# Performance work log

Measured on AMD Instinct MI355X. Metric: run time of the kernel, lower is better.

## Reference

```python
import jax, jax.numpy as jnp
import numpy as np
from functools import partial

BATCH, SEQ = 2, 2048
D_MODEL, D_INNER, D_XB = 2048, 4096, 1024
HEADDIM, D_STATE = 64, 64
NHEADS = D_INNER // HEADDIM      # 64
NKV = D_XB // HEADDIM            # 16
REP = NHEADS // NKV              # 4
INTER = 8192
EPS = 1e-5
D_IN_PROJ = D_INNER + D_XB + D_XB + D_INNER + NHEADS  # z, x, B, C, dt


def setup_inputs() -> dict:
    key = jax.random.key(0)
    ks = jax.random.split(key, 8)
    g = lambda k, shape, s: (jax.random.normal(k, shape, jnp.float32) * s)
    return {
        "hidden_states": g(ks[0], (BATCH, SEQ, D_MODEL), 1.0),
        "ln_w": jnp.ones((D_MODEL,), jnp.float32),
        "ln_b": jnp.zeros((D_MODEL,), jnp.float32),
        "in_proj_w": g(ks[1], (D_IN_PROJ, D_MODEL), 0.02),
        "dt_bias": jax.random.uniform(ks[2], (NHEADS,), jnp.float32, -4.0, 0.0),
        "A_log": jnp.log(jnp.arange(1, NHEADS + 1, dtype=jnp.float32)),
        "Dp": jnp.ones((NHEADS,), jnp.float32),
        "norm_w": jnp.ones((D_INNER,), jnp.float32),
        "out_proj_w": g(ks[3], (D_MODEL, D_INNER), 0.02),
        "fc1_w": g(ks[4], (INTER, D_MODEL), 0.02),
        "fc1_b": jnp.zeros((INTER,), jnp.float32),
        "fc2_w": g(ks[5], (D_MODEL, INTER), 0.02),
        "fc2_b": jnp.zeros((D_MODEL,), jnp.float32),
    }


def _layernorm(x, w, b):
    mu = x.mean(-1, keepdims=True)
    var = ((x - mu) ** 2).mean(-1, keepdims=True)
    return (x - mu) * jax.lax.rsqrt(var + EPS) * w + b


def _ssd_scan(xh, dt, A, Bh, Ch):
    # xh: (b,l,h,p)  dt: (b,l,h)  A: (h,)  Bh,Ch: (b,l,h,n)
    dA = jnp.exp(dt * A)  # (b,l,h) discrete decay
    to_l = lambda t: jnp.moveaxis(t, 1, 0)  # time-major for scan

    def step(state, inp):
        dA_t, dt_t, x_t, B_t, C_t = inp
        state = state * dA_t[:, :, None, None] + jnp.einsum(
            "bh,bhp,bhn->bhpn", dt_t, x_t, B_t)
        y = jnp.einsum("bhpn,bhn->bhp", state, C_t)
        return state, y

    state0 = jnp.zeros((xh.shape[0], NHEADS, HEADDIM, D_STATE), xh.dtype)
    _, ys = jax.lax.scan(step, state0, (to_l(dA), to_l(dt), to_l(xh), to_l(Bh), to_l(Ch)))
    return jnp.moveaxis(ys, 0, 1)  # (b,l,h,p)


def reference(hidden_states, ln_w, ln_b, in_proj_w, dt_bias, A_log, Dp,
              norm_w, out_proj_w, fc1_w, fc1_b, fc2_w, fc2_b):
    residual = hidden_states
    h = _layernorm(hidden_states, ln_w, ln_b)

    # ---- Mamba2 branch ----
    zxbcdt = h @ in_proj_w.T  # (b,l,D_IN_PROJ)
    z, x, Bm, Cm, dt = jnp.split(
        zxbcdt, np.cumsum([D_INNER, D_XB, D_XB, D_INNER]).tolist(), axis=-1)
    b, l = h.shape[0], h.shape[1]
    dt = jax.nn.softplus(dt + dt_bias)               # (b,l,nheads)
    A = -jnp.exp(A_log)                              # (nheads,)
    # GQA-style repeat of x (values) and B (keys) from NKV to NHEADS groups
    xh = jnp.repeat(x.reshape(b, l, NKV, HEADDIM), REP, axis=2)   # (b,l,h,p)
    Bh = jnp.repeat(Bm.reshape(b, l, NKV, D_STATE), REP, axis=2)  # (b,l,h,n)
    Ch = Cm.reshape(b, l, NHEADS, D_STATE)                        # (b,l,h,n)

    y = _ssd_scan(xh, dt, A, Bh, Ch) + Dp[None, None, :, None] * xh
    yf = y.reshape(b, l, D_INNER)
    # gated RMSNorm (norm_before_gate=False): gate first, then rmsnorm
    yf = yf * jax.nn.silu(z)
    yf = yf * jax.lax.rsqrt((yf * yf).mean(-1, keepdims=True) + EPS) * norm_w
    mamba_out = yf @ out_proj_w.T

    # ---- Phi MLP branch (parallel, shares the layernormed input) ----
    mlp = jax.nn.gelu(h @ fc1_w.T + fc1_b, approximate=True) @ fc2_w.T + fc2_b

    # resid_dropout is identity in eval mode
    return mamba_out + mlp + residual
```

## Files before the change

kernel.cpp:

```cpp
#include <hip/hip_runtime.h>
#include <hip/hip_bf16.h>

#define BATCH 2
#define SEQ   2048
#define DMODEL 2048
#define DINNER 4096
#define DXB   1024
#define NHEADS 64
#define NKV   16
#define HEADDIM 64
#define DSTATE 64
#define INTER 8192
#define DINPROJ 10304
#define ROWS  (BATCH*SEQ)
#define NC    32
#define EPSV  1e-5f

typedef short short8 __attribute__((ext_vector_type(8)));
typedef float f32x4 __attribute__((ext_vector_type(4)));

typedef const __attribute__((address_space(1))) unsigned int cg_u32;
typedef __attribute__((address_space(3))) unsigned int ls_u32;

static __device__ __forceinline__ void gll16(const void* g, void* l) {
    __builtin_amdgcn_global_load_lds((cg_u32*)g, (ls_u32*)l, 16, 0, 0);
}

static __device__ __forceinline__ unsigned short f2bf(float f) {
    unsigned int u = __float_as_uint(f);
    unsigned int r = (u + 0x7fffu + ((u >> 16) & 1u)) >> 16;
    return (unsigned short)r;
}
static __device__ __forceinline__ float bf2f(unsigned short h) {
    return __uint_as_float(((unsigned int)h) << 16);
}

__global__ __launch_bounds__(256) void convk(const float* __restrict__ in,
                                             unsigned short* __restrict__ out, int n4) {
    int stride = gridDim.x * blockDim.x;
    for (int i = blockIdx.x * blockDim.x + threadIdx.x; i < n4; i += stride) {
        float4 v = ((const float4*)in)[i];
        ushort4 o;
        o.x = f2bf(v.x); o.y = f2bf(v.y); o.z = f2bf(v.z); o.w = f2bf(v.w);
        ((ushort4*)out)[i] = o;
    }
}

__global__ __launch_bounds__(256) void ln_kernel(const float* __restrict__ x,
                                                 const float* __restrict__ w,
                                                 const float* __restrict__ b,
                                                 unsigned short* __restrict__ hout) {
    int row = blockIdx.x;
    int t = threadIdx.x;
    const float* xr = x + (size_t)row * DMODEL;
    float v[8];
    float4 v0 = *(const float4*)&xr[t * 8];
    float4 v1 = *(const float4*)&xr[t * 8 + 4];
    v[0]=v0.x; v[1]=v0.y; v[2]=v0.z; v[3]=v0.w; v[4]=v1.x; v[5]=v1.y; v[6]=v1.z; v[7]=v1.w;
    float s = 0.f, s2 = 0.f;
    #pragma unroll
    for (int i = 0; i < 8; ++i) { s += v[i]; s2 += v[i]*v[i]; }
    #pragma unroll
    for (int off = 1; off < 64; off <<= 1) { s += __shfl_xor(s, off); s2 += __shfl_xor(s2, off); }
    __shared__ float sa[4], sb[4];
    int lane = t & 63, wv = t >> 6;
    if (lane == 0) { sa[wv] = s; sb[wv] = s2; }
    __syncthreads();
    s = sa[0]+sa[1]+sa[2]+sa[3];
    s2 = sb[0]+sb[1]+sb[2]+sb[3];
    float mu = s / DMODEL;
    float var = s2 / DMODEL - mu * mu;
    float sc = rsqrtf(var + EPSV);
    unsigned short* ho = hout + (size_t)row * DMODEL + t * 8;
    #pragma unroll
    for (int i = 0; i < 8; ++i) {
        int d = t * 8 + i;
        ho[i] = f2bf((v[i] - mu) * sc * w[d] + b[d]);
    }
}

#define SLOTSZ 49152
template <int EPI>
__global__ __launch_bounds__(512, 2) void gemm_p(
    const unsigned short* __restrict__ A, const unsigned short* __restrict__ B,
    int M, int N, int K, int nby,
    float* __restrict__ outF, unsigned short* __restrict__ outH,
    const float* __restrict__ bias, const float* __restrict__ add1,
    const float* __restrict__ add2) {
    __shared__ __align__(16) char smem[3 * SLOTSZ];
    int t = threadIdx.x, lane = t & 63, w = t >> 6;
    int nwg = gridDim.x, cpx = nwg >> 3;
    int logical = (blockIdx.x & 7) * cpx + (blockIdx.x >> 3);
    int by = logical % nby, bx = logical / nby;
    int brow = by * 128, bcol = bx * 256;
    int wr = w >> 2, wc = w & 3;
    int wrb = wr * 64, wcb = wc * 64;

    int lr8 = lane >> 3;
    int lch = ((lane & 7) ^ lr8) << 3;
    const unsigned short* pa[2];
    #pragma unroll
    for (int j = 0; j < 2; ++j)
        pa[j] = A + (size_t)(brow + w * 16 + j * 8 + lr8) * K + lch;
    const unsigned short* pb[4];
    #pragma unroll
    for (int j = 0; j < 4; ++j) {
        int r = bcol + w * 32 + j * 8 + lr8;
        if (r > N - 1) r = N - 1;
        pb[j] = B + (size_t)r * K + lch;
    }
    auto stageA = [&](int slot, int j) {
        gll16(pa[j], smem + slot * SLOTSZ + (w * 16 + j * 8) * 128);
        pa[j] += 64;
    };
    auto stageB = [&](int slot, int j) {
        gll16(pb[j], smem + slot * SLOTSZ + 16384 + (w * 32 + j * 8) * 128);
        pb[j] += 64;
    };

    int arow = lane & 15;
    int swz0 = (((lane >> 4) ^ (lane & 7)) << 4);

    f32x4 acc[4][4] = {};
    const int NT = K >> 6;
    #pragma unroll
    for (int j = 0; j < 2; ++j) stageA(0, j);
    #pragma unroll
    for (int j = 0; j < 4; ++j) stageB(0, j);
    #pragma unroll
    for (int j = 0; j < 2; ++j) stageA(1, j);
    #pragma unroll
    for (int j = 0; j < 4; ++j) stageB(1, j);

    int slot = 0, slot2 = 2;
    for (int kt = 0; kt < NT; ++kt) {
        if (kt + 1 < NT) { asm volatile("s_waitcnt vmcnt(6)" ::: "memory"); }
        else             { asm volatile("s_waitcnt vmcnt(0)" ::: "memory"); }
        __builtin_amdgcn_s_barrier();
        asm volatile("" ::: "memory");
        const char* Ab = smem + slot * SLOTSZ;
        const char* Bb = Ab + 16384;
        bool st = (kt + 2 < NT);
        short8 af[4], bfv[4];
        #pragma unroll
        for (int f = 0; f < 4; ++f)
            af[f] = *(const short8*)(Ab + (wrb + f * 16 + arow) * 128 + swz0);
        #pragma unroll
        for (int n = 0; n < 4; ++n)
            bfv[n] = *(const short8*)(Bb + (wcb + n * 16 + arow) * 128 + swz0);
        if (st) { stageA(slot2, 0); stageA(slot2, 1); stageB(slot2, 0); }
        __builtin_amdgcn_s_setprio(1);
        #pragma unroll
        for (int f = 0; f < 4; ++f)
            #pragma unroll
            for (int n = 0; n < 4; ++n)
                acc[f][n] = __builtin_amdgcn_mfma_f32_16x16x32_bf16(af[f], bfv[n], acc[f][n], 0, 0, 0);
        __builtin_amdgcn_s_setprio(0);
        #pragma unroll
        for (int f = 0; f < 4; ++f)
            af[f] = *(const short8*)(Ab + (wrb + f * 16 + arow) * 128 + (swz0 ^ 64));
        #pragma unroll
        for (int n = 0; n < 4; ++n)
            bfv[n] = *(const short8*)(Bb + (wcb + n * 16 + arow) * 128 + (swz0 ^ 64));
        if (st) { stageB(slot2, 1); stageB(slot2, 2); stageB(slot2, 3); }
        __builtin_amdgcn_s_setprio(1);
        #pragma unroll
        for (int f = 0; f < 4; ++f)
            #pragma unroll
            for (int n = 0; n < 4; ++n)
                acc[f][n] = __builtin_amdgcn_mfma_f32_16x16x32_bf16(af[f], bfv[n], acc[f][n], 0, 0, 0);
        __builtin_amdgcn_s_setprio(0);
        slot  = (slot  == 2) ? 0 : slot + 1;
        slot2 = (slot2 == 2) ? 0 : slot2 + 1;
    }

    int rlane = (lane >> 4) << 2, clane = lane & 15;
    #pragma unroll
    for (int f = 0; f < 4; ++f) {
        #pragma unroll
        for (int n = 0; n < 4; ++n) {
            int col = bcol + wcb + n * 16 + clane;
            if (col < N) {
                #pragma unroll
                for (int j = 0; j < 4; ++j) {
                    int row = brow + wrb + f * 16 + rlane + j;
                    size_t idx = (size_t)row * N + col;
                    float v = acc[f][n][j];
                    if constexpr (EPI == 0) {
                        outF[idx] = v;
                    } else if constexpr (EPI == 1) {
                        v += bias[col];
                        float g = 0.5f * v * (1.f + tanhf(0.7978845608f * (v + 0.044715f * v * v * v)));
                        outH[idx] = f2bf(g);
                    } else if constexpr (EPI == 2) {
                        outF[idx] = v + bias[col] + add1[idx] + add2[idx];
                    } else {
                        outH[idx] = f2bf(v);
                    }
                }
            }
        }
    }
}

static __device__ __forceinline__ void mm64(const unsigned short* Al, const unsigned short* Bl,
                                            f32x4* acc, int w, int lane) {
    int lr = lane & 15, kg = (lane >> 4) << 3;
    #pragma unroll
    for (int ks = 0; ks < 2; ++ks) {
        short8 a = *(const short8*)&Al[(w * 16 + lr) * 64 + ks * 32 + kg];
        #pragma unroll
        for (int fn = 0; fn < 4; ++fn) {
            short8 bb = *(const short8*)&Bl[(fn * 16 + lr) * 64 + ks * 32 + kg];
            acc[fn] = __builtin_amdgcn_mfma_f32_16x16x32_bf16(a, bb, acc[fn], 0, 0, 0);
        }
    }
}

__global__ __launch_bounds__(256) void chunk_front(const unsigned short* __restrict__ zx,
                                                   const float* __restrict__ dt_bias,
                                                   const float* __restrict__ A_log,
                                                   float* __restrict__ pcum,
                                                   unsigned short* __restrict__ ybuf,
                                                   unsigned short* __restrict__ Sbuf) {
    __shared__ __align__(16) unsigned short Cs[64*64], Bsr[64*64], Btr[64*64],
                                            Xtr[64*64], Xw[64*64], Wsm[64*64];
    __shared__ float dts[64], clg[64];
    int t = threadIdx.x, lane = t & 63, w = t >> 6;
    int bid = blockIdx.x;
    int c = bid & 31, h = (bid >> 5) & 63, b = bid >> 11, g = h >> 2;
    int row0 = (b << 11) + (c << 6);

    if (t < 64) {
        float raw = bf2f(zx[(size_t)(row0 + t) * DINPROJ + 10240 + h]) + dt_bias[h];
        float dt = raw > 20.f ? raw : log1pf(expf(raw));
        dts[t] = dt;
        float v = dt * (-expf(A_log[h]));
        #pragma unroll
        for (int off = 1; off < 64; off <<= 1) {
            float o = __shfl_up(v, off);
            if (lane >= off) v += o;
        }
        clg[t] = v;
        pcum[(size_t)(row0 + t) * 64 + h] = expf(v);
    }
    ushort4 xr[4];
    #pragma unroll
    for (int i = 0; i < 4; ++i) {
        int q = i * 256 + t, s = q >> 4, d4 = (q & 15) << 2;
        const unsigned short* rp = zx + (size_t)(row0 + s) * DINPROJ;
        ushort4 cv = *(const ushort4*)&rp[6144 + h * 64 + d4];
        *(ushort4*)&Cs[s * 64 + d4] = cv;
        ushort4 bv = *(const ushort4*)&rp[5120 + g * 64 + d4];
        *(ushort4*)&Bsr[s * 64 + d4] = bv;
        Btr[(d4 + 0) * 64 + s] = bv.x; Btr[(d4 + 1) * 64 + s] = bv.y;
        Btr[(d4 + 2) * 64 + s] = bv.z; Btr[(d4 + 3) * 64 + s] = bv.w;
        ushort4 xv = *(const ushort4*)&rp[4096 + g * 64 + d4];
        Xtr[(d4 + 0) * 64 + s] = xv.x; Xtr[(d4 + 1) * 64 + s] = xv.y;
        Xtr[(d4 + 2) * 64 + s] = xv.z; Xtr[(d4 + 3) * 64 + s] = xv.w;
        xr[i] = xv;
    }
    __syncthreads();
    float cl63 = clg[63];
    #pragma unroll
    for (int i = 0; i < 4; ++i) {
        int q = i * 256 + t, s = q >> 4, d4 = (q & 15) << 2;
        float ws = dts[s] * expf(cl63 - clg[s]);
        Xw[(d4 + 0) * 64 + s] = f2bf(bf2f(xr[i].x) * ws);
        Xw[(d4 + 1) * 64 + s] = f2bf(bf2f(xr[i].y) * ws);
        Xw[(d4 + 2) * 64 + s] = f2bf(bf2f(xr[i].z) * ws);
        Xw[(d4 + 3) * 64 + s] = f2bf(bf2f(xr[i].w) * ws);
    }
    __syncthreads();
    f32x4 accG[4] = {};
    mm64(Cs, Bsr, accG, w, lane);
    int rl = (lane >> 4) << 2, cl = lane & 15;
    #pragma unroll
    for (int fn = 0; fn < 4; ++fn) {
        #pragma unroll
        for (int j = 0; j < 4; ++j) {
            int tr = w * 16 + rl + j, rc = fn * 16 + cl;
            float val = 0.f;
            if (rc <= tr) val = accG[fn][j] * expf(clg[tr] - clg[rc]) * dts[rc];
            Wsm[tr * 64 + rc] = f2bf(val);
        }
    }
    __syncthreads();
    f32x4 accY[4] = {};
    mm64(Wsm, Xtr, accY, w, lane);
    f32x4 accS[4] = {};
    mm64(Xw, Btr, accS, w, lane);
    size_t cb = (size_t)((((b << 6) + h) << 5) + c) * 4096;
    #pragma unroll
    for (int fn = 0; fn < 4; ++fn) {
        #pragma unroll
        for (int j = 0; j < 4; ++j) {
            int tr = w * 16 + rl + j, pc = fn * 16 + cl;
            ybuf[(size_t)(row0 + tr) * DINNER + h * 64 + pc] = f2bf(accY[fn][j]);
            Sbuf[cb + tr * 64 + pc] = f2bf(accS[fn][j]);
        }
    }
}

__global__ __launch_bounds__(256) void chunk_state(unsigned short* __restrict__ SH,
                                                   const float* __restrict__ pcum) {
    int b = blockIdx.x >> 6, h = blockIdx.x & 63, t = threadIdx.x;
    float H[16];
    #pragma unroll
    for (int j = 0; j < 16; ++j) H[j] = 0.f;
    for (int c = 0; c < NC; ++c) {
        size_t base = (size_t)((((b << 6) + h) << 5) + c) * 4096;
        float Tc = pcum[(size_t)((b << 11) + (c << 6) + 63) * 64 + h];
        #pragma unroll
        for (int j = 0; j < 16; ++j) {
            int e = j * 256 + t;
            unsigned short sv = SH[base + e];
            SH[base + e] = f2bf(H[j]);
            H[j] = H[j] * Tc + bf2f(sv);
        }
    }
}

__global__ __launch_bounds__(256) void chunk_back(const unsigned short* __restrict__ zx,
                                                  const unsigned short* __restrict__ SH,
                                                  const float* __restrict__ pcum,
                                                  const float* __restrict__ Dp,
                                                  unsigned short* __restrict__ ybuf) {
    __shared__ __align__(16) unsigned short Cs[64*64], Hs[64*64];
    __shared__ float ps[64];
    int t = threadIdx.x, lane = t & 63, w = t >> 6;
    int bid = blockIdx.x;
    int c = bid & 31, h = (bid >> 5) & 63, b = bid >> 11, g = h >> 2;
    int row0 = (b << 11) + (c << 6);
    size_t cb = (size_t)((((b << 6) + h) << 5) + c) * 4096;
    #pragma unroll
    for (int i = 0; i < 4; ++i) {
        int q = i * 256 + t, s = q >> 4, d4 = (q & 15) << 2;
        *(ushort4*)&Cs[s * 64 + d4] =
            *(const ushort4*)&zx[(size_t)(row0 + s) * DINPROJ + 6144 + h * 64 + d4];
        *(ushort4*)&Hs[s * 64 + d4] = *(const ushort4*)&SH[cb + s * 64 + d4];
    }
    if (t < 64) ps[t] = pcum[(size_t)(row0 + t) * 64 + h];
    __syncthreads();
    f32x4 acc[4] = {};
    mm64(Cs, Hs, acc, w, lane);
    float Dph = Dp[h];
    int rl = (lane >> 4) << 2, cl = lane & 15;
    #pragma unroll
    for (int fn = 0; fn < 4; ++fn) {
        #pragma unroll
        for (int j = 0; j < 4; ++j) {
            int tr = w * 16 + rl + j, pc = fn * 16 + cl;
            size_t yi = (size_t)(row0 + tr) * DINNER + h * 64 + pc;
            float xv = bf2f(zx[(size_t)(row0 + tr) * DINPROJ + 4096 + g * 64 + pc]);
            ybuf[yi] = f2bf(bf2f(ybuf[yi]) + acc[fn][j] * ps[tr] + Dph * xv);
        }
    }
}

__global__ __launch_bounds__(256) void gate_kernel(const unsigned short* __restrict__ y,
                                                   const unsigned short* __restrict__ zx,
                                                   const float* __restrict__ norm_w,
                                                   unsigned short* __restrict__ yf) {
    int row = blockIdx.x;
    int t = threadIdx.x;
    float v[16];
    float s2 = 0.f;
    #pragma unroll
    for (int i = 0; i < 16; ++i) {
        int d = i * 256 + t;
        float yv = bf2f(y[(size_t)row * DINNER + d]);
        float zv = bf2f(zx[(size_t)row * DINPROJ + d]);
        float gt = zv / (1.f + expf(-zv));
        v[i] = yv * gt;
        s2 += v[i] * v[i];
    }
    #pragma unroll
    for (int off = 1; off < 64; off <<= 1) s2 += __shfl_xor(s2, off);
    __shared__ float sb[4];
    int lane = t & 63, wv = t >> 6;
    if (lane == 0) sb[wv] = s2;
    __syncthreads();
    s2 = sb[0] + sb[1] + sb[2] + sb[3];
    float sc = rsqrtf(s2 / DINNER + EPSV);
    #pragma unroll
    for (int i = 0; i < 16; ++i) {
        int d = i * 256 + t;
        yf[(size_t)row * DINNER + d] = f2bf(v[i] * sc * norm_w[d]);
    }
}

extern "C" void kernel_launch(void* const* d_in, const int* in_sizes, int n_in,
                              void* d_out, int out_size, void* d_ws, size_t ws_size,
                              hipStream_t stream) {
    const float* hid   = (const float*)d_in[0];
    const float* ln_w  = (const float*)d_in[1];
    const float* ln_b  = (const float*)d_in[2];
    const float* w_inp = (const float*)d_in[3];
    const float* dtb   = (const float*)d_in[4];
    const float* A_log = (const float*)d_in[5];
    const float* Dp    = (const float*)d_in[6];
    const float* nw    = (const float*)d_in[7];
    const float* w_out = (const float*)d_in[8];
    const float* w_fc1 = (const float*)d_in[9];
    const float* fc1_b = (const float*)d_in[10];
    const float* w_fc2 = (const float*)d_in[11];
    const float* fc2_b = (const float*)d_in[12];

    char* ws = (char*)d_ws;
    size_t off = 0;
    auto alloc = [&](size_t bytes) { size_t o = off; off += (bytes + 255) & ~(size_t)255; return o; };
    size_t o_h    = alloc((size_t)ROWS * DMODEL * 2);
    size_t o_w    = alloc((size_t)DINPROJ * DMODEL * 2);
    size_t o_zx   = alloc((size_t)ROWS * DINPROJ * 2);
    size_t o_pc   = alloc((size_t)ROWS * NHEADS * 4);
    size_t o_y    = alloc((size_t)ROWS * DINNER * 2);
    size_t o_yf   = alloc((size_t)ROWS * DINNER * 2);
    size_t o_S    = alloc((size_t)BATCH * NHEADS * NC * HEADDIM * DSTATE * 2);

    unsigned short* h_bf  = (unsigned short*)(ws + o_h);
    unsigned short* wbuf  = (unsigned short*)(ws + o_w);
    unsigned short* zx    = (unsigned short*)(ws + o_zx);
    float* pcum           = (float*)(ws + o_pc);
    unsigned short* ybuf  = (unsigned short*)(ws + o_y);
    unsigned short* yf    = (unsigned short*)(ws + o_yf);
    unsigned short* Sbuf  = (unsigned short*)(ws + o_S);
    unsigned short* gelu  = (unsigned short*)(ws + o_zx);
    float* mamba          = (float*)(ws + o_y);
    float* outF           = (float*)d_out;

    ln_kernel<<<ROWS, 256, 0, stream>>>(hid, ln_w, ln_b, h_bf);
    convk<<<2048, 256, 0, stream>>>(w_inp, wbuf, (DINPROJ * DMODEL) / 4);
    gemm_p<3><<<41 * 32, 512, 0, stream>>>(
        h_bf, wbuf, ROWS, DINPROJ, DMODEL, 32, nullptr, zx, nullptr, nullptr, nullptr);
    chunk_front<<<BATCH * NHEADS * NC, 256, 0, stream>>>(zx, dtb, A_log, pcum, ybuf, Sbuf);
    chunk_state<<<BATCH * NHEADS, 256, 0, stream>>>(Sbuf, pcum);
    chunk_back<<<BATCH * NHEADS * NC, 256, 0, stream>>>(zx, Sbuf, pcum, Dp, ybuf);
    gate_kernel<<<ROWS, 256, 0, stream>>>(ybuf, zx, nw, yf);
    convk<<<2048, 256, 0, stream>>>(w_out, wbuf, (DMODEL * DINNER) / 4);
    gemm_p<0><<<8 * 32, 512, 0, stream>>>(
        yf, wbuf, ROWS, DMODEL, DINNER, 32, mamba, nullptr, nullptr, nullptr, nullptr);
    convk<<<2048, 256, 0, stream>>>(w_fc1, wbuf, (INTER * DMODEL) / 4);
    gemm_p<1><<<32 * 32, 512, 0, stream>>>(
        h_bf, wbuf, ROWS, INTER, DMODEL, 32, nullptr, gelu, fc1_b, nullptr, nullptr);
    convk<<<2048, 256, 0, stream>>>(w_fc2, wbuf, (DMODEL * INTER) / 4);
    gemm_p<2><<<8 * 32, 512, 0, stream>>>(
        gelu, wbuf, ROWS, DMODEL, INTER, 32, outF, nullptr, fc2_b, mamba, hid);
}
```

Before: 792.1 us.

## Fold weight conversions into earlier kernels and switch GEMM to 32x32 MFMA

Removes the four standalone fp32-to-bf16 weight conversion launches. Each conversion now runs as a grid-stride tail inside an earlier kernel (layernorm, the in_proj GEMM, chunk_front, the out_proj GEMM), writing into its own dedicated buffer. This saves launches and lets conversion overlap with tail effects, at the cost of more workspace and longer kernels. Separately, the GEMM inner loop moves from 16x16x32 to 32x32x16 bf16 MFMA with a matching fragment layout and epilogue, meant to cut LDS fragment reads per MFMA.

Measured after the change: 866.4 us. 9.4% more time.

```diff
diff --git a/kernel.cpp b/kernel.cpp
--- a/kernel.cpp
+++ b/kernel.cpp
@@ -18,6 +18,7 @@
 
 typedef short short8 __attribute__((ext_vector_type(8)));
 typedef float f32x4 __attribute__((ext_vector_type(4)));
+typedef float f32x16 __attribute__((ext_vector_type(16)));
 
 typedef const __attribute__((address_space(1))) unsigned int cg_u32;
 typedef __attribute__((address_space(3))) unsigned int ls_u32;
@@ -35,21 +36,24 @@
     return __uint_as_float(((unsigned int)h) << 16);
 }
 
-__global__ __launch_bounds__(256) void convk(const float* __restrict__ in,
-                                             unsigned short* __restrict__ out, int n4) {
-    int stride = gridDim.x * blockDim.x;
-    for (int i = blockIdx.x * blockDim.x + threadIdx.x; i < n4; i += stride) {
-        float4 v = ((const float4*)in)[i];
+static __device__ __forceinline__ void conv_gs(const float* __restrict__ src,
+                                               unsigned short* __restrict__ dst,
+                                               int n4, int gtid, int gstride) {
+    if (!src) return;
+    for (int i = gtid; i < n4; i += gstride) {
+        float4 v = ((const float4*)src)[i];
         ushort4 o;
         o.x = f2bf(v.x); o.y = f2bf(v.y); o.z = f2bf(v.z); o.w = f2bf(v.w);
-        ((ushort4*)out)[i] = o;
+        ((ushort4*)dst)[i] = o;
     }
 }
 
 __global__ __launch_bounds__(256) void ln_kernel(const float* __restrict__ x,
                                                  const float* __restrict__ w,
                                                  const float* __restrict__ b,
-                                                 unsigned short* __restrict__ hout) {
+                                                 unsigned short* __restrict__ hout,
+                                                 const float* __restrict__ csrc,
+                                                 unsigned short* __restrict__ cdst, int cn4) {
     int row = blockIdx.x;
     int t = threadIdx.x;
     const float* xr = x + (size_t)row * DMODEL;
@@ -77,6 +81,7 @@
         int d = t * 8 + i;
         ho[i] = f2bf((v[i] - mu) * sc * w[d] + b[d]);
     }
+    conv_gs(csrc, cdst, cn4, blockIdx.x * 256 + t, gridDim.x * 256);
 }
 
 #define SLOTSZ 49152
@@ -86,7 +91,8 @@
     int M, int N, int K, int nby,
     float* __restrict__ outF, unsigned short* __restrict__ outH,
     const float* __restrict__ bias, const float* __restrict__ add1,
-    const float* __restrict__ add2) {
+    const float* __restrict__ add2,
+    const float* __restrict__ csrc, unsigned short* __restrict__ cdst, int cn4) {
     __shared__ __align__(16) char smem[3 * SLOTSZ];
     int t = threadIdx.x, lane = t & 63, w = t >> 6;
     int nwg = gridDim.x, cpx = nwg >> 3;
@@ -118,10 +124,10 @@
         pb[j] += 64;
     };
 
-    int arow = lane & 15;
-    int swz0 = (((lane >> 4) ^ (lane & 7)) << 4);
-
-    f32x4 acc[4][4] = {};
+    int arow = lane & 31;
+    int khi = lane >> 5;
+
+    f32x16 acc[2][2] = {};
     const int NT = K >> 6;
     #pragma unroll
     for (int j = 0; j < 2; ++j) stageA(0, j);
@@ -141,51 +147,70 @@
         const char* Ab = smem + slot * SLOTSZ;
         const char* Bb = Ab + 16384;
         bool st = (kt + 2 < NT);
-        short8 af[4], bfv[4];
-        #pragma unroll
-        for (int f = 0; f < 4; ++f)
-            af[f] = *(const short8*)(Ab + (wrb + f * 16 + arow) * 128 + swz0);
-        #pragma unroll
-        for (int n = 0; n < 4; ++n)
-            bfv[n] = *(const short8*)(Bb + (wcb + n * 16 + arow) * 128 + swz0);
+        short8 af[2][2], bfv[2][2];
+        #pragma unroll
+        for (int ks = 0; ks < 2; ++ks) {
+            int chunk = (ks << 1) | khi;
+            #pragma unroll
+            for (int f = 0; f < 2; ++f) {
+                int r = wrb + f * 32 + arow;
+                af[ks][f] = *(const short8*)(Ab + r * 128 + ((chunk ^ (r & 7)) << 4));
+            }
+            #pragma unroll
+            for (int n = 0; n < 2; ++n) {
+                int r = wcb + n * 32 + arow;
+                bfv[ks][n] = *(const short8*)(Bb + r * 128 + ((chunk ^ (r & 7)) << 4));
+            }
+        }
         if (st) { stageA(slot2, 0); stageA(slot2, 1); stageB(slot2, 0); }
         __builtin_amdgcn_s_setprio(1);
         #pragma unroll
-        for (int f = 0; f < 4; ++f)
-            #pragma unroll
-            for (int n = 0; n < 4; ++n)
-                acc[f][n] = __builtin_amdgcn_mfma_f32_16x16x32_bf16(af[f], bfv[n], acc[f][n], 0, 0, 0);
+        for (int ks = 0; ks < 2; ++ks)
+            #pragma unroll
+            for (int f = 0; f < 2; ++f)
+                #pragma unroll
+                for (int n = 0; n < 2; ++n)
+                    acc[f][n] = __builtin_amdgcn_mfma_f32_32x32x16_bf16(af[ks][f], bfv[ks][n], acc[f][n], 0, 0, 0);
         __builtin_amdgcn_s_setprio(0);
         #pragma unroll
-        for (int f = 0; f < 4; ++f)
-            af[f] = *(const short8*)(Ab + (wrb + f * 16 + arow) * 128 + (swz0 ^ 64));
-        #pragma unroll
-        for (int n = 0; n < 4; ++n)
-            bfv[n] = *(const short8*)(Bb + (wcb + n * 16 + arow) * 128 + (swz0 ^ 64));
+        for (int ks = 0; ks < 2; ++ks) {
+            int chunk = ((ks + 2) << 1) | khi;
+            #pragma unroll
+            for (int f = 0; f < 2; ++f) {
+                int r = wrb + f * 32 + arow;
+                af[ks][f] = *(const short8*)(Ab + r * 128 + ((chunk ^ (r & 7)) << 4));
+            }
+            #pragma unroll
+            for (int n = 0; n < 2; ++n) {
+                int r = wcb + n * 32 + arow;
+                bfv[ks][n] = *(const short8*)(Bb + r * 128 + ((chunk ^ (r & 7)) << 4));
+            }
+        }
         if (st) { stageB(slot2, 1); stageB(slot2, 2); stageB(slot2, 3); }
         __builtin_amdgcn_s_setprio(1);
         #pragma unroll
-        for (int f = 0; f < 4; ++f)
-            #pragma unroll
-            for (int n = 0; n < 4; ++n)
-                acc[f][n] = __builtin_amdgcn_mfma_f32_16x16x32_bf16(af[f], bfv[n], acc[f][n], 0, 0, 0);
+        for (int ks = 0; ks < 2; ++ks)
+            #pragma unroll
+            for (int f = 0; f < 2; ++f)
+                #pragma unroll
+                for (int n = 0; n < 2; ++n)
+                    acc[f][n] = __builtin_amdgcn_mfma_f32_32x32x16_bf16(af[ks][f], bfv[ks][n], acc[f][n], 0, 0, 0);
         __builtin_amdgcn_s_setprio(0);
         slot  = (slot  == 2) ? 0 : slot + 1;
         slot2 = (slot2 == 2) ? 0 : slot2 + 1;
     }
 
-    int rlane = (lane >> 4) << 2, clane = lane & 15;
-    #pragma unroll
-    for (int f = 0; f < 4; ++f) {
-        #pragma unroll
-        for (int n = 0; n < 4; ++n) {
-            int col = bcol + wcb + n * 16 + clane;
+    #pragma unroll
+    for (int f = 0; f < 2; ++f) {
+        #pragma unroll
+        for (int n = 0; n < 2; ++n) {
+            int col = bcol + wcb + n * 32 + arow;
             if (col < N) {
                 #pragma unroll
-                for (int j = 0; j < 4; ++j) {
-                    int row = brow + wrb + f * 16 + rlane + j;
+                for (int reg = 0; reg < 16; ++reg) {
+                    int row = brow + wrb + f * 32 + (reg & 3) + ((reg >> 2) << 3) + (khi << 2);
                     size_t idx = (size_t)row * N + col;
-                    float v = acc[f][n][j];
+                    float v = acc[f][n][reg];
                     if constexpr (EPI == 0) {
                         outF[idx] = v;
                     } else if constexpr (EPI == 1) {
@@ -201,6 +226,7 @@
             }
         }
     }
+    conv_gs(csrc, cdst, cn4, (int)blockIdx.x * 512 + t, nwg * 512);
 }
 
 static __device__ __forceinline__ void mm64(const unsigned short* Al, const unsigned short* Bl,
@@ -222,7 +248,9 @@
                                                    const float* __restrict__ A_log,
                                                    float* __restrict__ pcum,
                                                    unsigned short* __restrict__ ybuf,
-                                                   unsigned short* __restrict__ Sbuf) {
+                                                   unsigned short* __restrict__ Sbuf,
+                                                   const float* __restrict__ csrc,
+                                                   unsigned short* __restrict__ cdst, int cn4) {
     __shared__ __align__(16) unsigned short Cs[64*64], Bsr[64*64], Btr[64*64],
                                             Xtr[64*64], Xw[64*64], Wsm[64*64];
     __shared__ float dts[64], clg[64];
@@ -300,6 +328,7 @@
             Sbuf[cb + tr * 64 + pc] = f2bf(accS[fn][j]);
         }
     }
+    conv_gs(csrc, cdst, cn4, bid * 256 + t, (int)gridDim.x * 256);
 }
 
 __global__ __launch_bounds__(256) void chunk_state(unsigned short* __restrict__ SH,
@@ -411,7 +440,10 @@
     size_t off = 0;
     auto alloc = [&](size_t bytes) { size_t o = off; off += (bytes + 255) & ~(size_t)255; return o; };
     size_t o_h    = alloc((size_t)ROWS * DMODEL * 2);
-    size_t o_w    = alloc((size_t)DINPROJ * DMODEL * 2);
+    size_t o_wi   = alloc((size_t)DINPROJ * DMODEL * 2);
+    size_t o_wo   = alloc((size_t)DMODEL * DINNER * 2);
+    size_t o_wf1  = alloc((size_t)INTER * DMODEL * 2);
+    size_t o_wf2  = alloc((size_t)DMODEL * INTER * 2);
     size_t o_zx   = alloc((size_t)ROWS * DINPROJ * 2);
     size_t o_pc   = alloc((size_t)ROWS * NHEADS * 4);
     size_t o_y    = alloc((size_t)ROWS * DINNER * 2);
@@ -419,7 +451,10 @@
     size_t o_S    = alloc((size_t)BATCH * NHEADS * NC * HEADDIM * DSTATE * 2);
 
     unsigned short* h_bf  = (unsigned short*)(ws + o_h);
-    unsigned short* wbuf  = (unsigned short*)(ws + o_w);
+    unsigned short* wbi   = (unsigned short*)(ws + o_wi);
+    unsigned short* wbo   = (unsigned short*)(ws + o_wo);
+    unsigned short* wbf1  = (unsigned short*)(ws + o_wf1);
+    unsigned short* wbf2  = (unsigned short*)(ws + o_wf2);
     unsigned short* zx    = (unsigned short*)(ws + o_zx);
     float* pcum           = (float*)(ws + o_pc);
     unsigned short* ybuf  = (unsigned short*)(ws + o_y);
@@ -429,21 +464,23 @@
     float* mamba          = (float*)(ws + o_y);
     float* outF           = (float*)d_out;
 
-    ln_kernel<<<ROWS, 256, 0, stream>>>(hid, ln_w, ln_b, h_bf);
-    convk<<<2048, 256, 0, stream>>>(w_inp, wbuf, (DINPROJ * DMODEL) / 4);
+    ln_kernel<<<ROWS, 256, 0, stream>>>(hid, ln_w, ln_b, h_bf,
+                                        w_inp, wbi, (DINPROJ * DMODEL) / 4);
     gemm_p<3><<<41 * 32, 512, 0, stream>>>(
-        h_bf, wbuf, ROWS, DINPROJ, DMODEL, 32, nullptr, zx, nullptr, nullptr, nullptr);
-    chunk_front<<<BATCH * NHEADS * NC, 256, 0, stream>>>(zx, dtb, A_log, pcum, ybuf, Sbuf);
+        h_bf, wbi, ROWS, DINPROJ, DMODEL, 32, nullptr, zx, nullptr, nullptr, nullptr,
+        w_out, wbo, (DMODEL * DINNER) / 4);
+    chunk_front<<<BATCH * NHEADS * NC, 256, 0, stream>>>(zx, dtb, A_log, pcum, ybuf, Sbuf,
+                                                         w_fc1, wbf1, (INTER * DMODEL) / 4);
     chunk_state<<<BATCH * NHEADS, 256, 0, stream>>>(Sbuf, pcum);
     chunk_back<<<BATCH * NHEADS * NC, 256, 0, stream>>>(zx, Sbuf, pcum, Dp, ybuf);
     gate_kernel<<<ROWS, 256, 0, stream>>>(ybuf, zx, nw, yf);
-    convk<<<2048, 256, 0, stream>>>(w_out, wbuf, (DMODEL * DINNER) / 4);
     gemm_p<0><<<8 * 32, 512, 0, stream>>>(
-        yf, wbuf, ROWS, DMODEL, DINNER, 32, mamba, nullptr, nullptr, nullptr, nullptr);
-    convk<<<2048, 256, 0, stream>>>(w_fc1, wbuf, (INTER * DMODEL) / 4);
+        yf, wbo, ROWS, DMODEL, DINNER, 32, mamba, nullptr, nullptr, nullptr, nullptr,
+        w_fc2, wbf2, (DMODEL * INTER) / 4);
     gemm_p<1><<<32 * 32, 512, 0, stream>>>(
-        h_bf, wbuf, ROWS, INTER, DMODEL, 32, nullptr, gelu, fc1_b, nullptr, nullptr);
-    convk<<<2048, 256, 0, stream>>>(w_fc2, wbuf, (DMODEL * INTER) / 4);
+        h_bf, wbf1, ROWS, INTER, DMODEL, 32, nullptr, gelu, fc1_b, nullptr, nullptr,
+        nullptr, nullptr, 0);
     gemm_p<2><<<8 * 32, 512, 0, stream>>>(
-        gelu, wbuf, ROWS, DMODEL, INTER, 32, outF, nullptr, fc2_b, mamba, hid);
-}
+        gelu, wbf2, ROWS, DMODEL, INTER, 32, outF, nullptr, fc2_b, mamba, hid,
+        nullptr, nullptr, 0);
+}
```
